# Optimization experiments

Measured on AMD Instinct MI355X. Metric: run time of the kernel, lower is better.

The kernel has to match this reference:

```python
import jax, jax.numpy as jnp
import numpy as np

B, S, H, L = 32, 512, 1024, 2


def setup_inputs() -> dict:
    key = jax.random.key(0)
    k0, k1, k2, k3, k4 = jax.random.split(key, 5)
    s = 1.0 / np.sqrt(H)  # mimic nn.Linear uniform fan-in scale (avoids gate saturation)
    x = jax.random.normal(k0, (B, S, H), dtype=jnp.float32)
    h = jnp.zeros((B, L, H), dtype=jnp.float32)
    # stacked gate weights, gate order along 3H axis: [r, z, n]
    Wi_w = jax.random.normal(k1, (L, 3 * H, H), dtype=jnp.float32) * s
    Wi_b = jax.random.normal(k2, (L, 3 * H), dtype=jnp.float32) * s
    Wh_w = jax.random.normal(k3, (L, 3 * H, H), dtype=jnp.float32) * s
    Wh_b = jax.random.normal(k4, (L, 3 * H), dtype=jnp.float32) * s
    return {"x": x, "h": h, "Wi_w": Wi_w, "Wi_b": Wi_b, "Wh_w": Wh_w, "Wh_b": Wh_b}


def _gru_layer(inp, h0, wi, bi, wh, bh):
    # inp: [B,S,D], h0: [B,H], wi: [3H,D], wh: [3H,H]
    xi = jnp.einsum('bsd,gd->bsg', inp, wi) + bi  # precompute input gates [B,S,3H]

    def step(h_prev, xt):
        hg = h_prev @ wh.T + bh                   # [B,3H]
        xr, xz, xn = jnp.split(xt, 3, axis=-1)
        hr, hz, hn = jnp.split(hg, 3, axis=-1)
        r = jax.nn.sigmoid(xr + hr)
        z = jax.nn.sigmoid(xz + hz)
        n = jnp.tanh(xn + r * hn)
        h_new = z * h_prev + (1.0 - z) * n
        return h_new, h_new

    hT, ys = jax.lax.scan(step, h0, jnp.swapaxes(xi, 0, 1))  # scan over time
    return jnp.swapaxes(ys, 0, 1), hT  # y:[B,S,H], hT:[B,H]


def reference(x, h, Wi_w, Wi_b, Wh_w, Wh_b):
    out = x
    finals = []
    for l in range(Wi_w.shape[0]):
        out, hT = _gru_layer(out, h[:, l, :], Wi_w[l], Wi_b[l], Wh_w[l], Wh_b[l])
        finals.append(hT)
    return out, jnp.stack(finals, axis=1)  # y:[B,S,H], final_h:[B,L,H]
```

## Files before the change

### kernel.cpp

```cpp
#include <hip/hip_runtime.h>

#define HD    1024
#define SEQ   512
#define NB    32
#define G3    3072
#define MR    16384
#define PBLK2 512

__device__ __forceinline__ float sigmoidf_(float v) { return 1.0f / (1.0f + __expf(-v)); }

#define DPP_XADD(acc, ctrl, rmask)                                              \
    acc += __int_as_float(__builtin_amdgcn_update_dpp(                          \
        0, __float_as_int(acc), ctrl, rmask, 0xf, false))

__device__ __forceinline__ float wave_reduce_sum(float a)
{
    DPP_XADD(a, 0xB1,  0xF);
    DPP_XADD(a, 0x4E,  0xF);
    DPP_XADD(a, 0x141, 0xF);
    DPP_XADD(a, 0x140, 0xF);
    DPP_XADD(a, 0x142, 0xA);
    DPP_XADD(a, 0x143, 0xC);
    return __int_as_float(__builtin_amdgcn_readlane(__float_as_int(a), 63));
}

__global__ __launch_bounds__(256, 2) void gemm_xi(const float* __restrict__ A,
                                                  const float* __restrict__ W,
                                                  const float* __restrict__ bias,
                                                  float* __restrict__ C)
{
    __shared__ float As[16][132];
    __shared__ float Ws[16][132];

    const int t  = threadIdx.x;
    const int m0 = blockIdx.x * 128;
    const int n0 = blockIdx.y * 128;
    const int tx = t & 15;
    const int ty = t >> 4;
    const int lr = t >> 2;
    const int kq = t & 3;

    float acc[8][8];
#pragma unroll
    for (int i = 0; i < 8; ++i)
#pragma unroll
        for (int j = 0; j < 8; ++j) acc[i][j] = 0.0f;

    const float* Ap = A + (size_t)(m0 + lr) * HD + kq * 4;
    const float* Wp = W + (size_t)(n0 + lr) * HD + kq * 4;

    for (int k0 = 0; k0 < HD; k0 += 16) {
        float4 a0 = *(const float4*)(Ap + k0);
        float4 a1 = *(const float4*)(Ap + (size_t)64 * HD + k0);
        float4 w0 = *(const float4*)(Wp + k0);
        float4 w1 = *(const float4*)(Wp + (size_t)64 * HD + k0);
        __syncthreads();
        As[kq*4+0][lr]    = a0.x; As[kq*4+1][lr]    = a0.y;
        As[kq*4+2][lr]    = a0.z; As[kq*4+3][lr]    = a0.w;
        As[kq*4+0][lr+64] = a1.x; As[kq*4+1][lr+64] = a1.y;
        As[kq*4+2][lr+64] = a1.z; As[kq*4+3][lr+64] = a1.w;
        Ws[kq*4+0][lr]    = w0.x; Ws[kq*4+1][lr]    = w0.y;
        Ws[kq*4+2][lr]    = w0.z; Ws[kq*4+3][lr]    = w0.w;
        Ws[kq*4+0][lr+64] = w1.x; Ws[kq*4+1][lr+64] = w1.y;
        Ws[kq*4+2][lr+64] = w1.z; Ws[kq*4+3][lr+64] = w1.w;
        __syncthreads();
#pragma unroll
        for (int k = 0; k < 16; ++k) {
            float4 av0 = *(const float4*)(&As[k][ty*8]);
            float4 av1 = *(const float4*)(&As[k][ty*8+4]);
            float4 bv0 = *(const float4*)(&Ws[k][tx*8]);
            float4 bv1 = *(const float4*)(&Ws[k][tx*8+4]);
            float a[8]  = {av0.x, av0.y, av0.z, av0.w, av1.x, av1.y, av1.z, av1.w};
            float bb[8] = {bv0.x, bv0.y, bv0.z, bv0.w, bv1.x, bv1.y, bv1.z, bv1.w};
#pragma unroll
            for (int i = 0; i < 8; ++i)
#pragma unroll
                for (int j = 0; j < 8; ++j)
                    acc[i][j] = fmaf(a[i], bb[j], acc[i][j]);
        }
    }

    float4 bb0 = *(const float4*)(bias + n0 + tx*8);
    float4 bb1 = *(const float4*)(bias + n0 + tx*8 + 4);
    const float bv[8] = {bb0.x, bb0.y, bb0.z, bb0.w, bb1.x, bb1.y, bb1.z, bb1.w};
#pragma unroll
    for (int i = 0; i < 8; ++i) {
        float* crow = C + (size_t)(m0 + ty*8 + i) * G3 + n0 + tx*8;
        float4 o0 = {acc[i][0]+bv[0], acc[i][1]+bv[1], acc[i][2]+bv[2], acc[i][3]+bv[3]};
        float4 o1 = {acc[i][4]+bv[4], acc[i][5]+bv[5], acc[i][6]+bv[6], acc[i][7]+bv[7]};
        *(float4*)(crow)     = o0;
        *(float4*)(crow + 4) = o1;
    }
}

__global__ __launch_bounds__(256, 2) void gru_persist2(const float* __restrict__ xi,
                                                       const float* __restrict__ Wh,
                                                       const float* __restrict__ bh,
                                                       const float* __restrict__ h0,
                                                       float* __restrict__ y,
                                                       float* __restrict__ fin,
                                                       float* __restrict__ hb0,
                                                       float* __restrict__ hb1,
                                                       unsigned* __restrict__ cnt,
                                                       int layer)
{
    __shared__ float  hs[16 * HD];
    __shared__ float4 xis[3][16];

    const int tid  = threadIdx.x;
    const int bk   = blockIdx.x;
    const int w    = tid >> 6;
    const int lane = tid & 63;
    const int bg   = bk & 1;
    const int jq   = bk >> 1;
    const int j    = jq * 4 + w;
    const int b0   = bg * 16;

    float4 w0[4], w1[4], w2[4];
#pragma unroll
    for (int c = 0; c < 4; ++c) {
        w0[c] = *(const float4*)(Wh + (size_t)j          * HD + 256*c + 4*lane);
        w1[c] = *(const float4*)(Wh + (size_t)(HD + j)   * HD + 256*c + 4*lane);
        w2[c] = *(const float4*)(Wh + (size_t)(2*HD + j) * HD + 256*c + 4*lane);
    }
    const float bhr = bh[j], bhz = bh[HD + j], bhn = bh[2*HD + j];

    for (int t = 0; t < SEQ; ++t) {
        if (t == 0) {
            const int r = tid >> 4, pc = tid & 15;
            const float* src = h0 + (size_t)(b0 + r) * (2*HD) + (size_t)layer * HD;
#pragma unroll
            for (int c = 0; c < 16; ++c) {
                const int f4 = pc * 16 + c;
                *(float4*)(hs + (size_t)r * HD + f4 * 4) =
                    *(const float4*)(src + f4 * 4);
            }
        } else {
            const float* src = ((t & 1) ? hb0 : hb1) + (size_t)b0 * HD;
#pragma unroll
            for (int c = 0; c < 16; ++c) {
                const int f4 = c * 256 + tid;
                *(float4*)(hs + f4 * 4) = *(const float4*)(src + f4 * 4);
            }
        }
        if (tid < 48) {
            const int g = tid >> 4, bl = tid & 15;
            xis[g][bl] = *(const float4*)(xi + ((size_t)(b0 + bl) * SEQ + t) * G3
                                             + g * HD + jq * 4);
        }
        __syncthreads();

        float* hbw = (t & 1) ? hb1 : hb0;

#pragma unroll 4
        for (int b = 0; b < 16; ++b) {
            const float* hp = hs + (size_t)b * HD;
            float ar = 0.f, az = 0.f, an = 0.f;
#pragma unroll
            for (int c = 0; c < 4; ++c) {
                float4 hq = *(const float4*)(hp + 256*c + 4*lane);
                ar = fmaf(w0[c].x, hq.x, ar); ar = fmaf(w0[c].y, hq.y, ar);
                ar = fmaf(w0[c].z, hq.z, ar); ar = fmaf(w0[c].w, hq.w, ar);
                az = fmaf(w1[c].x, hq.x, az); az = fmaf(w1[c].y, hq.y, az);
                az = fmaf(w1[c].z, hq.z, az); az = fmaf(w1[c].w, hq.w, az);
                an = fmaf(w2[c].x, hq.x, an); an = fmaf(w2[c].y, hq.y, an);
                an = fmaf(w2[c].z, hq.z, an); an = fmaf(w2[c].w, hq.w, an);
            }
            const float sr = wave_reduce_sum(ar);
            const float sz = wave_reduce_sum(az);
            const float sn = wave_reduce_sum(an);

            const float xr = ((const float*)&xis[0][b])[w];
            const float xz = ((const float*)&xis[1][b])[w];
            const float xn = ((const float*)&xis[2][b])[w];

            const float rr  = sigmoidf_(xr + sr + bhr);
            const float zz  = sigmoidf_(xz + sz + bhz);
            const float hpv = hp[j];
            const float e   = __expf(2.0f * (xn + rr * (sn + bhn)));
            const float nn  = 1.0f - 2.0f / (e + 1.0f);
            const float hnew = zz * hpv + (1.0f - zz) * nn;

            if (lane == 0) {
                __hip_atomic_store(hbw + (size_t)(b0 + b) * HD + j, hnew,
                                   __ATOMIC_RELAXED, __HIP_MEMORY_SCOPE_AGENT);
                y[((size_t)(b0 + b) * SEQ + t) * HD + j] = hnew;
                if (t == SEQ - 1)
                    fin[((size_t)(b0 + b) * 2 + layer) * HD + j] = hnew;
            }
        }

        if (t < SEQ - 1) {
            __syncthreads();
            if (tid == 0)
                __hip_atomic_fetch_add(cnt + (bk & 31) * 16, 1u,
                                       __ATOMIC_RELAXED, __HIP_MEMORY_SCOPE_AGENT);
            if (tid < 64) {
                const unsigned tgt = 16u * (unsigned)(t + 1);
                for (;;) {
                    unsigned v = tgt;
                    if (lane < 32)
                        v = __hip_atomic_load(cnt + lane * 16, __ATOMIC_RELAXED,
                                              __HIP_MEMORY_SCOPE_AGENT);
                    if (__all((int)(v >= tgt))) break;
                    __builtin_amdgcn_s_sleep(2);
                }
                __builtin_amdgcn_fence(__ATOMIC_ACQUIRE, "agent");
            }
            __syncthreads();
        }
    }
}

template <bool USE_XI>
__global__ __launch_bounds__(256) void gru_step(const float* __restrict__ xi,
                                                const float* __restrict__ xsrc,
                                                const float* __restrict__ Wi,
                                                const float* __restrict__ bi,
                                                const float* __restrict__ Wh,
                                                const float* __restrict__ bh,
                                                const float* __restrict__ hprev,
                                                float* __restrict__ hnext,
                                                float* __restrict__ y,
                                                int t)
{
    const int tid = threadIdx.x;
    const int b   = tid >> 3;
    const int jc  = tid & 7;
    const int j   = blockIdx.x * 8 + jc;

    const float* hp = hprev + (size_t)b * HD;
    const float* wr = Wh + (size_t)j * HD;
    const float* wz = Wh + (size_t)(HD + j) * HD;
    const float* wn = Wh + (size_t)(2*HD + j) * HD;

    float4 ar = {0,0,0,0}, az = {0,0,0,0}, an = {0,0,0,0};
#pragma unroll 4
    for (int k = 0; k < HD; k += 4) {
        float4 h4 = *(const float4*)(hp + k);
        float4 r4 = *(const float4*)(wr + k);
        float4 z4 = *(const float4*)(wz + k);
        float4 n4 = *(const float4*)(wn + k);
        ar.x = fmaf(h4.x, r4.x, ar.x); ar.y = fmaf(h4.y, r4.y, ar.y);
        ar.z = fmaf(h4.z, r4.z, ar.z); ar.w = fmaf(h4.w, r4.w, ar.w);
        az.x = fmaf(h4.x, z4.x, az.x); az.y = fmaf(h4.y, z4.y, az.y);
        az.z = fmaf(h4.z, z4.z, az.z); az.w = fmaf(h4.w, z4.w, az.w);
        an.x = fmaf(h4.x, n4.x, an.x); an.y = fmaf(h4.y, n4.y, an.y);
        an.z = fmaf(h4.z, n4.z, an.z); an.w = fmaf(h4.w, n4.w, an.w);
    }
    float dr = (ar.x + ar.y) + (ar.z + ar.w);
    float dz = (az.x + az.y) + (az.z + az.w);
    float dn = (an.x + an.y) + (an.z + an.w);

    const size_t row = (size_t)b * SEQ + t;
    float xr, xz, xn;
    if (USE_XI) {
        const float* xrow = xi + row * G3;
        xr = xrow[j]; xz = xrow[HD + j]; xn = xrow[2*HD + j];
    } else {
        const float* xp = xsrc + row * HD;
        const float* ur = Wi + (size_t)j * HD;
        const float* uz = Wi + (size_t)(HD + j) * HD;
        const float* un = Wi + (size_t)(2*HD + j) * HD;
        float4 xar = {0,0,0,0}, xaz = {0,0,0,0}, xan = {0,0,0,0};
#pragma unroll 4
        for (int k = 0; k < HD; k += 4) {
            float4 x4 = *(const float4*)(xp + k);
            float4 r4 = *(const float4*)(ur + k);
            float4 z4 = *(const float4*)(uz + k);
            float4 n4 = *(const float4*)(un + k);
            xar.x = fmaf(x4.x, r4.x, xar.x); xar.y = fmaf(x4.y, r4.y, xar.y);
            xar.z = fmaf(x4.z, r4.z, xar.z); xar.w = fmaf(x4.w, r4.w, xar.w);
            xaz.x = fmaf(x4.x, z4.x, xaz.x); xaz.y = fmaf(x4.y, z4.y, xaz.y);
            xaz.z = fmaf(x4.z, z4.z, xaz.z); xaz.w = fmaf(x4.w, z4.w, xaz.w);
            xan.x = fmaf(x4.x, n4.x, xan.x); xan.y = fmaf(x4.y, n4.y, xan.y);
            xan.z = fmaf(x4.z, n4.z, xan.z); xan.w = fmaf(x4.w, n4.w, xan.w);
        }
        xr = (xar.x + xar.y) + (xar.z + xar.w) + bi[j];
        xz = (xaz.x + xaz.y) + (xaz.z + xaz.w) + bi[HD + j];
        xn = (xan.x + xan.y) + (xan.z + xan.w) + bi[2*HD + j];
    }

    float hr = dr + bh[j];
    float hz = dz + bh[HD + j];
    float hn = dn + bh[2*HD + j];
    float r  = sigmoidf_(xr + hr);
    float z  = sigmoidf_(xz + hz);
    float n  = tanhf(xn + r * hn);
    float hpv  = hp[j];
    float hnew = z * hpv + (1.0f - z) * n;

    hnext[(size_t)b * HD + j] = hnew;
    y[row * HD + j]           = hnew;
}

__global__ __launch_bounds__(256) void copy_h(float* __restrict__ dst, int dstride,
                                              const float* __restrict__ src, int sstride)
{
    const int b = blockIdx.x;
    const int t = threadIdx.x;
    *(float4*)(dst + (size_t)b * dstride + t * 4) =
        *(const float4*)(src + (size_t)b * sstride + t * 4);
}

extern "C" void kernel_launch(void* const* d_in, const int* in_sizes, int n_in,
                              void* d_out, int out_size, void* d_ws, size_t ws_size,
                              hipStream_t stream)
{
    const float* x  = (const float*)d_in[0];
    const float* h0 = (const float*)d_in[1];
    const float* Wi = (const float*)d_in[2];
    const float* bi = (const float*)d_in[3];
    const float* Wh = (const float*)d_in[4];
    const float* bh = (const float*)d_in[5];

    float* y   = (float*)d_out;
    float* fin = y + (size_t)MR * HD;

    const size_t xi_elems   = (size_t)MR * G3;
    const size_t hbuf_elems = (size_t)NB * HD;
    const size_t need_persist = 4096 + (xi_elems + 2 * hbuf_elems) * sizeof(float);

    if (ws_size >= need_persist) {
        unsigned* counters = (unsigned*)d_ws;
        float* xi  = (float*)((char*)d_ws + 4096);
        float* hb0 = xi + xi_elems;
        float* hb1 = hb0 + hbuf_elems;
        hipMemsetAsync(d_ws, 0, 4096, stream);

        for (int l = 0; l < 2; ++l) {
            const float* src  = (l == 0) ? x : (const float*)y;
            const float* Wi_l = Wi + (size_t)l * G3 * HD;
            const float* bi_l = bi + (size_t)l * G3;
            const float* Wh_l = Wh + (size_t)l * G3 * HD;
            const float* bh_l = bh + (size_t)l * G3;

            gemm_xi<<<dim3(128, 24), 256, 0, stream>>>(src, Wi_l, bi_l, xi);
            gru_persist2<<<PBLK2, 256, 0, stream>>>(xi, Wh_l, bh_l, h0, y, fin,
                                                    hb0, hb1, counters + l * 512, l);
        }
        return;
    }

    float* xi = nullptr;
    float* hA;
    if (ws_size >= (xi_elems + 2 * hbuf_elems) * sizeof(float)) {
        xi = (float*)d_ws;
        hA = xi + xi_elems;
    } else {
        hA = (float*)d_ws;
    }
    float* hB = hA + hbuf_elems;

    for (int l = 0; l < 2; ++l) {
        const float* src = (l == 0) ? x : (const float*)y;
        const float* Wi_l = Wi + (size_t)l * G3 * HD;
        const float* bi_l = bi + (size_t)l * G3;
        const float* Wh_l = Wh + (size_t)l * G3 * HD;
        const float* bh_l = bh + (size_t)l * G3;

        if (xi != nullptr)
            gemm_xi<<<dim3(128, 24), 256, 0, stream>>>(src, Wi_l, bi_l, xi);

        copy_h<<<NB, 256, 0, stream>>>(hA, HD, h0 + (size_t)l * HD, 2 * HD);

        float* hp = hA;
        float* hn = hB;
        for (int tt = 0; tt < SEQ; ++tt) {
            if (xi != nullptr)
                gru_step<true><<<128, 256, 0, stream>>>(xi, src, Wi_l, bi_l, Wh_l, bh_l,
                                                        hp, hn, y, tt);
            else
                gru_step<false><<<128, 256, 0, stream>>>(nullptr, src, Wi_l, bi_l, Wh_l, bh_l,
                                                         hp, hn, y, tt);
            float* tmp = hp; hp = hn; hn = tmp;
        }
        copy_h<<<NB, 256, 0, stream>>>(fin + (size_t)l * HD, 2 * HD, hp, HD);
    }
}
```

Measured before the change: 20.38 ms.

## Use one 512-thread block per CU covering all batches in persistent GRU

The persistent recurrent kernel moves from 512 blocks of 256 threads, each covering 16 batches, to 256 blocks of 512 threads that each cover all 32 batches for 4 hidden units. Within a block, pairs of waves split the batch dimension in half. This halves the number of blocks in the per-step grid-wide barrier, and the barrier target is adjusted to match. In exchange each block stages the full 128KB hidden state into LDS every step, which relies on the larger LDS per CU, and each CU runs a single block.

```diff
diff --git a/kernel.cpp b/kernel.cpp
--- a/kernel.cpp
+++ b/kernel.cpp
@@ -5,7 +5,7 @@
 #define NB    32
 #define G3    3072
 #define MR    16384
-#define PBLK2 512
+#define PBLK3 256
 
 __device__ __forceinline__ float sigmoidf_(float v) { return 1.0f / (1.0f + __expf(-v)); }
 
@@ -93,7 +93,7 @@
     }
 }
 
-__global__ __launch_bounds__(256, 2) void gru_persist2(const float* __restrict__ xi,
+__global__ __launch_bounds__(512, 1) void gru_persist3(const float* __restrict__ xi,
                                                        const float* __restrict__ Wh,
                                                        const float* __restrict__ bh,
                                                        const float* __restrict__ h0,
@@ -104,17 +104,16 @@
                                                        unsigned* __restrict__ cnt,
                                                        int layer)
 {
-    __shared__ float  hs[16 * HD];
-    __shared__ float4 xis[3][16];
+    __shared__ float  hs[NB * HD];
+    __shared__ float4 xis[3][NB];
 
     const int tid  = threadIdx.x;
     const int bk   = blockIdx.x;
     const int w    = tid >> 6;
     const int lane = tid & 63;
-    const int bg   = bk & 1;
-    const int jq   = bk >> 1;
-    const int j    = jq * 4 + w;
-    const int b0   = bg * 16;
+    const int jc   = w >> 1;
+    const int half = w & 1;
+    const int j    = bk * 4 + jc;
 
     float4 w0[4], w1[4], w2[4];
 #pragma unroll
@@ -128,32 +127,33 @@
     for (int t = 0; t < SEQ; ++t) {
         if (t == 0) {
             const int r = tid >> 4, pc = tid & 15;
-            const float* src = h0 + (size_t)(b0 + r) * (2*HD) + (size_t)layer * HD;
-#pragma unroll
-            for (int c = 0; c < 16; ++c) {
-                const int f4 = pc * 16 + c;
+            const float* src = h0 + (size_t)r * (2*HD) + (size_t)layer * HD;
+#pragma unroll
+            for (int cc = 0; cc < 16; ++cc) {
+                const int f4 = pc * 16 + cc;
                 *(float4*)(hs + (size_t)r * HD + f4 * 4) =
                     *(const float4*)(src + f4 * 4);
             }
         } else {
-            const float* src = ((t & 1) ? hb0 : hb1) + (size_t)b0 * HD;
+            const float* src = (t & 1) ? hb0 : hb1;
 #pragma unroll
             for (int c = 0; c < 16; ++c) {
-                const int f4 = c * 256 + tid;
+                const int f4 = c * 512 + tid;
                 *(float4*)(hs + f4 * 4) = *(const float4*)(src + f4 * 4);
             }
         }
-        if (tid < 48) {
-            const int g = tid >> 4, bl = tid & 15;
-            xis[g][bl] = *(const float4*)(xi + ((size_t)(b0 + bl) * SEQ + t) * G3
-                                             + g * HD + jq * 4);
+        if (tid < 96) {
+            const int g = tid >> 5, bl = tid & 31;
+            xis[g][bl] = *(const float4*)(xi + ((size_t)bl * SEQ + t) * G3
+                                             + g * HD + bk * 4);
         }
         __syncthreads();
 
         float* hbw = (t & 1) ? hb1 : hb0;
 
 #pragma unroll 4
-        for (int b = 0; b < 16; ++b) {
+        for (int i = 0; i < 16; ++i) {
+            const int b = half * 16 + i;
             const float* hp = hs + (size_t)b * HD;
             float ar = 0.f, az = 0.f, an = 0.f;
 #pragma unroll
@@ -170,9 +170,9 @@
             const float sz = wave_reduce_sum(az);
             const float sn = wave_reduce_sum(an);
 
-            const float xr = ((const float*)&xis[0][b])[w];
-            const float xz = ((const float*)&xis[1][b])[w];
-            const float xn = ((const float*)&xis[2][b])[w];
+            const float xr = ((const float*)&xis[0][b])[jc];
+            const float xz = ((const float*)&xis[1][b])[jc];
+            const float xn = ((const float*)&xis[2][b])[jc];
 
             const float rr  = sigmoidf_(xr + sr + bhr);
             const float zz  = sigmoidf_(xz + sz + bhz);
@@ -182,11 +182,11 @@
             const float hnew = zz * hpv + (1.0f - zz) * nn;
 
             if (lane == 0) {
-                __hip_atomic_store(hbw + (size_t)(b0 + b) * HD + j, hnew,
+                __hip_atomic_store(hbw + (size_t)b * HD + j, hnew,
                                    __ATOMIC_RELAXED, __HIP_MEMORY_SCOPE_AGENT);
-                y[((size_t)(b0 + b) * SEQ + t) * HD + j] = hnew;
+                y[((size_t)b * SEQ + t) * HD + j] = hnew;
                 if (t == SEQ - 1)
-                    fin[((size_t)(b0 + b) * 2 + layer) * HD + j] = hnew;
+                    fin[((size_t)b * 2 + layer) * HD + j] = hnew;
             }
         }
 
@@ -196,7 +196,7 @@
                 __hip_atomic_fetch_add(cnt + (bk & 31) * 16, 1u,
                                        __ATOMIC_RELAXED, __HIP_MEMORY_SCOPE_AGENT);
             if (tid < 64) {
-                const unsigned tgt = 16u * (unsigned)(t + 1);
+                const unsigned tgt = 8u * (unsigned)(t + 1);
                 for (;;) {
                     unsigned v = tgt;
                     if (lane < 32)
@@ -336,7 +336,7 @@
             const float* bh_l = bh + (size_t)l * G3;
 
             gemm_xi<<<dim3(128, 24), 256, 0, stream>>>(src, Wi_l, bi_l, xi);
-            gru_persist2<<<PBLK2, 256, 0, stream>>>(xi, Wh_l, bh_l, h0, y, fin,
+            gru_persist3<<<PBLK3, 512, 0, stream>>>(xi, Wh_l, bh_l, h0, y, fin,
                                                     hb0, hb1, counters + l * 512, l);
         }
         return;
```

After: 18.51 ms. -9.2%, faster.
